# Performance work log

Hardware: AMD Instinct MI355X
Metric: run time of the kernel (lower is better)

## Reference

```python
import jax, jax.numpy as jnp
import numpy as np

C = 1024  # in_channels
B, SQ, SKV = 4, 2048, 2048


def setup_inputs() -> dict:
    key = jax.random.key(0)
    ks = jax.random.split(key, 10)
    s = 1.0 / np.sqrt(C)
    return {
        "x": jax.random.normal(ks[0], (B, SQ, C), jnp.float32),
        "content_embeddings": jax.random.normal(ks[1], (B, SKV, C), jnp.float32),
        "Wq": jax.random.normal(ks[2], (C, C), jnp.float32) * s,
        "bq": jnp.zeros((C,), jnp.float32),
        "Wk": jax.random.normal(ks[3], (C, C), jnp.float32) * s,
        "bk": jnp.zeros((C,), jnp.float32),
        "Wv": jax.random.normal(ks[4], (C, C), jnp.float32) * s,
        "bv": jnp.zeros((C,), jnp.float32),
        "Wo": jax.random.normal(ks[5], (C, C), jnp.float32) * s,
        "bo": jnp.zeros((C,), jnp.float32),
    }


def reference(x, content_embeddings, Wq, bq, Wk, bk, Wv, bv, Wo, bo):
    # torch Linear: y = x @ W.T + b
    queries = x @ Wq.T + bq                    # [B, SQ, C]
    keys = content_embeddings @ Wk.T + bk      # [B, SKV, C]
    values = content_embeddings @ Wv.T + bv    # [B, SKV, C]
    scale = 1.0 / jnp.sqrt(jnp.asarray(C, x.dtype))
    scores = jnp.einsum("bqc,bkc->bqk", queries, keys) * scale  # [B, SQ, SKV]
    attn = jax.nn.softmax(scores, axis=-1)
    attended = jnp.einsum("bqk,bkc->bqc", attn, values)         # [B, SQ, C]
    out = x + attended
    return out @ Wo.T + bo
```

## Files before the change

### kernel.cpp

```cpp
#include <hip/hip_runtime.h>


typedef __attribute__((ext_vector_type(8))) short short8;
typedef __attribute__((ext_vector_type(8))) unsigned short ushort8;
typedef __attribute__((ext_vector_type(4))) unsigned short ushort4v;
typedef __attribute__((ext_vector_type(4))) float f32x4;

__device__ __forceinline__ float b2f(unsigned short u) {
  union { unsigned int i; float f; } x;
  x.i = ((unsigned int)u) << 16;
  return x.f;
}
__device__ __forceinline__ unsigned short f2b(float f) {
  union { float f; unsigned int i; } x;
  x.f = f;
  unsigned int i = x.i;
  i += 0x7fffu + ((i >> 16) & 1u);
  return (unsigned short)(i >> 16);
}

__device__ __forceinline__ void async_copy16(const void* g, void* l) {
  __builtin_amdgcn_global_load_lds(
      (const __attribute__((address_space(1))) unsigned int*)g,
      (__attribute__((address_space(3))) unsigned int*)l, 16, 0, 0);
}

__global__ void detect_fmt(const unsigned short* __restrict__ x, int* flag) {
  __shared__ int cnt;
  if (threadIdx.x == 0) cnt = 0;
  __syncthreads();
  int c = 0;
  for (int i = threadIdx.x * 2; i < 8192; i += 512) {
    unsigned e = (x[i] >> 7) & 0xFF;
    if (e >= 0x90) ++c;
  }
  atomicAdd(&cnt, c);
  __syncthreads();
  if (threadIdx.x == 0) *flag = (cnt > 64) ? 1 : 0;
}

struct CvtArgs { const void* src[10]; };

__global__ __launch_bounds__(256) void convert_all(
    CvtArgs a, unsigned short* __restrict__ dst, const int* __restrict__ flag) {
  const bool f32 = (*flag != 0);
  const long nchunk = 2621952;
  for (long c = blockIdx.x * 256L + threadIdx.x; c < nchunk;
       c += 1024L * 256) {
    const long flat = c * 8;
    int t; long off;
    if      (flat < 8388608)  { t = 0; off = 0; }
    else if (flat < 16777216) { t = 1; off = 8388608; }
    else if (flat < 17825792) { t = 2; off = 16777216; }
    else if (flat < 17826816) { t = 3; off = 17825792; }
    else if (flat < 18875392) { t = 4; off = 17826816; }
    else if (flat < 18876416) { t = 5; off = 18875392; }
    else if (flat < 19924992) { t = 6; off = 18876416; }
    else if (flat < 19926016) { t = 7; off = 19924992; }
    else if (flat < 20974592) { t = 8; off = 19926016; }
    else                      { t = 9; off = 20974592; }
    const long li = flat - off;
    if (f32) {
      const float* s = (const float*)a.src[t] + li;
      const f32x4 lo = *(const f32x4*)s;
      const f32x4 hi = *(const f32x4*)(s + 4);
      ushort8 o;
      o[0] = f2b(lo[0]); o[1] = f2b(lo[1]); o[2] = f2b(lo[2]); o[3] = f2b(lo[3]);
      o[4] = f2b(hi[0]); o[5] = f2b(hi[1]); o[6] = f2b(hi[2]); o[7] = f2b(hi[3]);
      *(ushort8*)(dst + flat) = o;
    } else {
      *(ushort8*)(dst + flat) =
          *(const ushort8*)((const unsigned short*)a.src[t] + li);
    }
  }
}

#define MODE_BIAS 0
#define MODE_RES  2
#define MODE_SB   3
#define MODE_OUT  4

__device__ __forceinline__ void xcd_swizzle(int gx, int gy, int& bx, int& by) {
  const int L = blockIdx.y * gx + blockIdx.x;
  const int r = L & 7, m = L >> 3;
  bx = m % gx;
  by = r * (gy >> 3) + m / gx;
}

template <int MODE, int KU>
__device__ __forceinline__ void gemm_core(
    const unsigned short* __restrict__ A, const unsigned short* __restrict__ B,
    void* __restrict__ C, const unsigned short* __restrict__ bias,
    const unsigned short* __restrict__ Res, const int* __restrict__ flg,
    int N, int K, float scale, int bx, int by, int vt) {
  __shared__ __align__(16) unsigned short As[KU * 128 * 32];
  __shared__ __align__(16) unsigned short Bs[KU * 128 * 32];
  const int tid = threadIdx.x;
  const int wave = tid >> 6, lane = tid & 63;
  const int wm = wave >> 1, wn = wave & 1;
  const int quad = lane >> 4, lrow = lane & 15;

  const long arow0 = (long)by * 128 + (tid >> 2);
  const long brow0 = (long)bx * 128 + (tid >> 2);
  const int cstg = (tid & 3) * 8;
  const unsigned short* ag0 = A + arow0 * K + cstg;
  const unsigned short* ag1 = ag0 + 64L * K;
  const unsigned short* bg0 = B + brow0 * K + cstg;
  const unsigned short* bg1 = bg0 + 64L * K;
  char* lA0 = (char*)As + tid * 16;
  char* lA1 = (char*)As + (256 + tid) * 16;
  char* lB0 = (char*)Bs + tid * 16;
  char* lB1 = (char*)Bs + (256 + tid) * 16;

  f32x4 acc[4][4];
#pragma unroll
  for (int i = 0; i < 4; ++i)
#pragma unroll
    for (int j = 0; j < 4; ++j) acc[i][j] = (f32x4){0.f, 0.f, 0.f, 0.f};

  for (int kt = 0; kt < K; kt += 32 * KU) {
#pragma unroll
    for (int u = 0; u < KU; ++u) {
      async_copy16(ag0 + kt + u * 32, lA0 + u * 8192);
      async_copy16(ag1 + kt + u * 32, lA1 + u * 8192);
      async_copy16(bg0 + kt + u * 32, lB0 + u * 8192);
      async_copy16(bg1 + kt + u * 32, lB1 + u * 8192);
    }
    __syncthreads();
#pragma unroll
    for (int u = 0; u < KU; ++u) {
      const unsigned short* Au = As + u * 4096;
      const unsigned short* Bu = Bs + u * 4096;
      short8 af[4], bfr[4];
#pragma unroll
      for (int i = 0; i < 4; ++i)
        af[i] = *(const short8*)(Au + (wm * 64 + i * 16 + lrow) * 32 + quad * 8);
#pragma unroll
      for (int j = 0; j < 4; ++j)
        bfr[j] =
            *(const short8*)(Bu + (wn * 64 + j * 16 + lrow) * 32 + quad * 8);
#pragma unroll
      for (int i = 0; i < 4; ++i)
#pragma unroll
        for (int j = 0; j < 4; ++j)
          acc[i][j] = __builtin_amdgcn_mfma_f32_16x16x32_bf16(
              af[i], bfr[j], acc[i][j], 0, 0, 0);
    }
    __syncthreads();
  }

  const bool f32out = (MODE == MODE_OUT) ? (*flg != 0) : false;
#pragma unroll
  for (int i = 0; i < 4; ++i) {
    const long row = (long)by * 128 + wm * 64 + i * 16 + quad * 4;
#pragma unroll
    for (int j = 0; j < 4; ++j) {
      const long col = (long)bx * 128 + wn * 64 + j * 16 + lrow;
      if (MODE == MODE_BIAS && vt) {
        const float bb = b2f(bias[col]);
        ushort4v pk;
#pragma unroll
        for (int r = 0; r < 4; ++r) pk[r] = f2b(acc[i][j][r] + bb);
        const long b = row >> 11, kvr = row & 2047;
        *(ushort4v*)((unsigned short*)C + b * 2097152 + col * 2048 + kvr) = pk;
        continue;
      }
#pragma unroll
      for (int r = 0; r < 4; ++r) {
        const float v = acc[i][j][r];
        const long idx = (row + r) * N + col;
        if (MODE == MODE_BIAS) {
          ((unsigned short*)C)[idx] = f2b(v + b2f(bias[col]));
        } else if (MODE == MODE_SB) {
          ((unsigned short*)C)[idx] = f2b(v * scale);
        } else if (MODE == MODE_RES) {
          ((unsigned short*)C)[idx] = f2b(v + b2f(Res[idx]));
        } else {
          const float o = v + b2f(bias[col]);
          if (f32out) ((float*)C)[idx] = o;
          else        ((unsigned short*)C)[idx] = f2b(o);
        }
      }
    }
  }
}

template <int MODE, int KU>
__global__ __launch_bounds__(256, 2) void gemm_nt(
    const unsigned short* __restrict__ A, const unsigned short* __restrict__ B,
    void* __restrict__ C, const unsigned short* __restrict__ bias,
    const unsigned short* __restrict__ Res, const int* __restrict__ flg,
    int N, int K, float scale, long sA, long sB, long sC, long sR) {
  const int bz = blockIdx.z;
  int bx, by;
  xcd_swizzle(gridDim.x, gridDim.y, bx, by);
  const unsigned short* Rb = (MODE == MODE_RES) ? Res + bz * sR : nullptr;
  void* Cb = (MODE == MODE_OUT) ? (void*)((char*)C)
                                : (void*)((unsigned short*)C + bz * sC);
  gemm_core<MODE, KU>(A + bz * sA, B + bz * sB, Cb, bias, Rb, flg, N, K, scale,
                      bx, by, 0);
}

template <int MODE>
__device__ __forceinline__ void gemm256_core(
    const unsigned short* __restrict__ A, const unsigned short* __restrict__ B,
    void* __restrict__ C, const unsigned short* __restrict__ bias,
    const unsigned short* __restrict__ Res, const int* __restrict__ flg,
    int N, int K, float scale, int bx, int by, int vt) {
  __shared__ __align__(16) unsigned short lds[65536];
  const int tid = threadIdx.x;
  const int wave = tid >> 6, lane = tid & 63;
  const int wm = wave >> 2, wn = wave & 3;
  const int quad = lane >> 4, lrow = lane & 15;
  const int NT = K >> 6;

  const int srow = tid >> 3;
  const int sch = (tid & 7) ^ (srow & 7);
  const unsigned short* gA = A + (long)(by * 256 + srow) * K + sch * 8;
  const unsigned short* gB = B + (long)(bx * 256 + srow) * K + sch * 8;
  char* const ldst = (char*)lds + tid * 16;

  auto stageA = [&](int ts, int h) {
    const unsigned short* g = gA + (long)h * 128 * K + ts * 64;
    char* l = ldst + (ts & 1) * 32768 + h * 16384;
    async_copy16(g, l);
    async_copy16(g + (long)64 * K, l + 8192);
  };
  auto stageB = [&](int ts, int h) {
    const unsigned short* g = gB + (long)h * 128 * K + ts * 64;
    char* l = ldst + 65536 + (ts & 1) * 32768 + h * 16384;
    async_copy16(g, l);
    async_copy16(g + (long)64 * K, l + 8192);
  };

  const int chk0 = ((quad) ^ (lrow & 7)) << 3;
  const int chk1 = ((4 + quad) ^ (lrow & 7)) << 3;

  f32x4 acc[8][4];
#pragma unroll
  for (int i = 0; i < 8; ++i)
#pragma unroll
    for (int j = 0; j < 4; ++j) acc[i][j] = (f32x4){0.f, 0.f, 0.f, 0.f};

  stageB(0, 0); stageB(0, 1); stageA(0, 0); stageA(0, 1);
  stageB(1, 0); stageB(1, 1);
  asm volatile("s_waitcnt vmcnt(4)" ::: "memory");
  __builtin_amdgcn_s_barrier();

  for (int t = 0; t < NT; ++t) {
    const unsigned short* Au = lds + (t & 1) * 16384 + (wm * 128 + lrow) * 64;
    const unsigned short* Bu =
        lds + 32768 + (t & 1) * 16384 + (wn * 64 + lrow) * 64;
    short8 a[4][2], blo[2][2], bhi[2][2];

#pragma unroll
    for (int i = 0; i < 4; ++i) {
      a[i][0] = *(const short8*)(Au + i * 1024 + chk0);
      a[i][1] = *(const short8*)(Au + i * 1024 + chk1);
    }
#pragma unroll
    for (int j = 0; j < 2; ++j) {
      blo[j][0] = *(const short8*)(Bu + j * 1024 + chk0);
      blo[j][1] = *(const short8*)(Bu + j * 1024 + chk1);
    }
    if (t + 1 < NT) stageA(t + 1, 0);
    __builtin_amdgcn_s_barrier();
    asm volatile("s_waitcnt lgkmcnt(0)" ::: "memory");
    __builtin_amdgcn_sched_barrier(0);
    __builtin_amdgcn_s_setprio(1);
#pragma unroll
    for (int i = 0; i < 4; ++i)
#pragma unroll
      for (int j = 0; j < 2; ++j) {
        acc[i][j] = __builtin_amdgcn_mfma_f32_16x16x32_bf16(
            a[i][0], blo[j][0], acc[i][j], 0, 0, 0);
        acc[i][j] = __builtin_amdgcn_mfma_f32_16x16x32_bf16(
            a[i][1], blo[j][1], acc[i][j], 0, 0, 0);
      }
    __builtin_amdgcn_s_setprio(0);
    __builtin_amdgcn_s_barrier();

#pragma unroll
    for (int j = 0; j < 2; ++j) {
      bhi[j][0] = *(const short8*)(Bu + (j + 2) * 1024 + chk0);
      bhi[j][1] = *(const short8*)(Bu + (j + 2) * 1024 + chk1);
    }
    if (t + 1 < NT) stageA(t + 1, 1);
    __builtin_amdgcn_s_barrier();
    asm volatile("s_waitcnt lgkmcnt(0)" ::: "memory");
    __builtin_amdgcn_sched_barrier(0);
    __builtin_amdgcn_s_setprio(1);
#pragma unroll
    for (int i = 0; i < 4; ++i)
#pragma unroll
      for (int j = 0; j < 2; ++j) {
        acc[i][j + 2] = __builtin_amdgcn_mfma_f32_16x16x32_bf16(
            a[i][0], bhi[j][0], acc[i][j + 2], 0, 0, 0);
        acc[i][j + 2] = __builtin_amdgcn_mfma_f32_16x16x32_bf16(
            a[i][1], bhi[j][1], acc[i][j + 2], 0, 0, 0);
      }
    __builtin_amdgcn_s_setprio(0);
    __builtin_amdgcn_s_barrier();

#pragma unroll
    for (int i = 0; i < 4; ++i) {
      a[i][0] = *(const short8*)(Au + (i + 4) * 1024 + chk0);
      a[i][1] = *(const short8*)(Au + (i + 4) * 1024 + chk1);
    }
    if (t + 2 < NT) stageB(t + 2, 0);
    __builtin_amdgcn_s_barrier();
    asm volatile("s_waitcnt lgkmcnt(0)" ::: "memory");
    __builtin_amdgcn_sched_barrier(0);
    __builtin_amdgcn_s_setprio(1);
#pragma unroll
    for (int i = 0; i < 4; ++i)
#pragma unroll
      for (int j = 0; j < 2; ++j) {
        acc[i + 4][j + 2] = __builtin_amdgcn_mfma_f32_16x16x32_bf16(
            a[i][0], bhi[j][0], acc[i + 4][j + 2], 0, 0, 0);
        acc[i + 4][j + 2] = __builtin_amdgcn_mfma_f32_16x16x32_bf16(
            a[i][1], bhi[j][1], acc[i + 4][j + 2], 0, 0, 0);
      }
    __builtin_amdgcn_s_setprio(0);
    __builtin_amdgcn_s_barrier();

    if (t + 2 < NT) stageB(t + 2, 1);
    __builtin_amdgcn_s_barrier();
    __builtin_amdgcn_s_setprio(1);
#pragma unroll
    for (int i = 0; i < 4; ++i)
#pragma unroll
      for (int j = 0; j < 2; ++j) {
        acc[i + 4][j] = __builtin_amdgcn_mfma_f32_16x16x32_bf16(
            a[i][0], blo[j][0], acc[i + 4][j], 0, 0, 0);
        acc[i + 4][j] = __builtin_amdgcn_mfma_f32_16x16x32_bf16(
            a[i][1], blo[j][1], acc[i + 4][j], 0, 0, 0);
      }
    __builtin_amdgcn_s_setprio(0);
    if (t + 2 < NT) {
      asm volatile("s_waitcnt vmcnt(4)" ::: "memory");
    } else {
      asm volatile("s_waitcnt vmcnt(0)" ::: "memory");
    }
    __builtin_amdgcn_s_barrier();
  }

  const bool f32out = (MODE == MODE_OUT) ? (*flg != 0) : false;
  float bb[4];
  if (MODE == MODE_BIAS || MODE == MODE_OUT) {
#pragma unroll
    for (int j = 0; j < 4; ++j)
      bb[j] = b2f(bias[(long)bx * 256 + wn * 64 + j * 16 + lrow]);
  }
#pragma unroll
  for (int i = 0; i < 8; ++i) {
    const long row = (long)by * 256 + wm * 128 + i * 16 + quad * 4;
#pragma unroll
    for (int j = 0; j < 4; ++j) {
      const long col = (long)bx * 256 + wn * 64 + j * 16 + lrow;
      if (MODE == MODE_BIAS && vt) {
        ushort4v pk;
#pragma unroll
        for (int r = 0; r < 4; ++r) pk[r] = f2b(acc[i][j][r] + bb[j]);
        const long b = row >> 11, kvr = row & 2047;
        *(ushort4v*)((unsigned short*)C + b * 2097152 + col * 2048 + kvr) = pk;
        continue;
      }
#pragma unroll
      for (int r = 0; r < 4; ++r) {
        const float v = acc[i][j][r];
        const long idx = (row + r) * N + col;
        if (MODE == MODE_BIAS) {
          ((unsigned short*)C)[idx] = f2b(v + bb[j]);
        } else if (MODE == MODE_SB) {
          ((unsigned short*)C)[idx] = f2b(v * scale);
        } else if (MODE == MODE_RES) {
          ((unsigned short*)C)[idx] = f2b(v + b2f(Res[idx]));
        } else {
          const float o = v + bb[j];
          if (f32out) ((float*)C)[idx] = o;
          else        ((unsigned short*)C)[idx] = f2b(o);
        }
      }
    }
  }
}

template <int MODE>
__global__ __launch_bounds__(512, 2) void gemm_nt256(
    const unsigned short* __restrict__ A, const unsigned short* __restrict__ B,
    void* __restrict__ C, const unsigned short* __restrict__ bias,
    const unsigned short* __restrict__ Res, const int* __restrict__ flg,
    int N, int K, float scale, long sA, long sB, long sC, long sR) {
  const int bz = blockIdx.z;
  int bx, by;
  xcd_swizzle(gridDim.x, gridDim.y, bx, by);
  const unsigned short* Rb = (MODE == MODE_RES) ? Res + bz * sR : nullptr;
  void* Cb = (MODE == MODE_OUT) ? (void*)((char*)C)
                                : (void*)((unsigned short*)C + bz * sC);
  gemm256_core<MODE>(A + bz * sA, B + bz * sB, Cb, bias, Rb, flg, N, K, scale,
                     bx, by, 0);
}

struct QkvArgs {
  const unsigned short* A[3];
  const unsigned short* B[3];
  unsigned short* C[3];
  const unsigned short* bias[3];
};
__global__ __launch_bounds__(512, 2) void gemm_qkv(QkvArgs a, int N, int K) {
  const int z = blockIdx.z;
  int bx, by;
  xcd_swizzle(gridDim.x, gridDim.y, bx, by);
  gemm256_core<MODE_BIAS>(a.A[z], a.B[z], a.C[z], a.bias[z], nullptr, nullptr,
                          N, K, 1.f, bx, by, z == 2 ? 1 : 0);
}

__global__ __launch_bounds__(256) void softmax_rows(
    unsigned short* __restrict__ SP) {
  unsigned short* s = SP + blockIdx.x * 2048L;
  const int tid = threadIdx.x;
  const ushort8 raw = *(const ushort8*)(s + tid * 8);
  float v[8];
#pragma unroll
  for (int i = 0; i < 8; ++i) v[i] = b2f(raw[i]);
  float m = v[0];
#pragma unroll
  for (int i = 1; i < 8; ++i) m = fmaxf(m, v[i]);
#pragma unroll
  for (int off = 32; off > 0; off >>= 1) m = fmaxf(m, __shfl_xor(m, off));
  __shared__ float redm[4], reds[4];
  if ((tid & 63) == 0) redm[tid >> 6] = m;
  __syncthreads();
  m = fmaxf(fmaxf(redm[0], redm[1]), fmaxf(redm[2], redm[3]));
  float sum = 0.f;
#pragma unroll
  for (int i = 0; i < 8; ++i) {
    v[i] = __expf(v[i] - m);
    sum += v[i];
  }
#pragma unroll
  for (int off = 32; off > 0; off >>= 1) sum += __shfl_xor(sum, off);
  if ((tid & 63) == 0) reds[tid >> 6] = sum;
  __syncthreads();
  sum = reds[0] + reds[1] + reds[2] + reds[3];
  const float inv = 1.0f / sum;
  ushort8 o;
#pragma unroll
  for (int i = 0; i < 8; ++i) o[i] = f2b(v[i] * inv);
  *(ushort8*)(s + tid * 8) = o;
}

extern "C" void kernel_launch(void* const* d_in, const int* in_sizes, int n_in,
                              void* d_out, int out_size, void* d_ws,
                              size_t ws_size, hipStream_t stream) {
  char* ws = (char*)d_ws;
  const long MB = 1 << 20;
  unsigned short* C0  = (unsigned short*)ws;
  unsigned short* xb  = C0;
  unsigned short* ceb = C0 + 8388608;
  unsigned short* Wqb = C0 + 16777216;
  unsigned short* bqb = C0 + 17825792;
  unsigned short* Wkb = C0 + 17826816;
  unsigned short* bkb = C0 + 18875392;
  unsigned short* Wvb = C0 + 18876416;
  unsigned short* bvb = C0 + 19924992;
  unsigned short* Wob = C0 + 19926016;
  unsigned short* bob = C0 + 20974592;
  int*            flg = (int*)(ws + 41 * MB);
  unsigned short* Q   = (unsigned short*)(ws + 42 * MB);
  unsigned short* Kp  = (unsigned short*)(ws + 58 * MB);
  unsigned short* Vt  = (unsigned short*)(ws + 74 * MB);
  unsigned short* S   = (unsigned short*)(ws + 90 * MB);
  unsigned short* Ar  = Kp;

  const float scale = 0.03125f;

  detect_fmt<<<dim3(1), dim3(256), 0, stream>>>((const unsigned short*)d_in[0],
                                                flg);
  CvtArgs ca;
  for (int i = 0; i < 10; ++i) ca.src[i] = d_in[i];
  convert_all<<<dim3(1024), dim3(256), 0, stream>>>(ca, C0, flg);

  QkvArgs qa;
  qa.A[0] = xb;  qa.A[1] = ceb; qa.A[2] = ceb;
  qa.B[0] = Wqb; qa.B[1] = Wkb; qa.B[2] = Wvb;
  qa.C[0] = Q;   qa.C[1] = Kp;  qa.C[2] = Vt;
  qa.bias[0] = bqb; qa.bias[1] = bkb; qa.bias[2] = bvb;
  gemm_qkv<<<dim3(4, 32, 3), dim3(512), 0, stream>>>(qa, 1024, 1024);

  gemm_nt256<MODE_SB><<<dim3(8, 8, 4), dim3(512), 0, stream>>>(
      Q, Kp, S, nullptr, nullptr, nullptr, 2048, 1024, scale,
      2048L * 1024, 2048L * 1024, 2048L * 2048, 0);

  softmax_rows<<<dim3(8192), dim3(256), 0, stream>>>(S);

  gemm_nt<MODE_RES, 2><<<dim3(8, 16, 4), dim3(256), 0, stream>>>(
      S, Vt, Ar, nullptr, xb, nullptr, 1024, 2048, 1.f,
      2048L * 2048, 1024L * 2048, 2048L * 1024, 2048L * 1024);

  gemm_nt<MODE_OUT, 2><<<dim3(8, 64, 1), dim3(256), 0, stream>>>(
      Ar, Wob, d_out, bob, nullptr, flg, 1024, 1024, 1.f, 0, 0, 0, 0);
}
```

Measured before the change: 330.8 us.

## Restructure GEMM main loop to one prefetch stage with K-split LDS fragments

Replaces the 8-phase ping-pong main loop, which had many block barriers and a two-tile-deep B prefetch, with a single-stage prefetch. All A and B tiles for step t+1 are issued at once, and each step ends with one vmcnt(0) wait and a barrier. LDS fragment reads are split by K half, and partial lgkmcnt waits let MFMAs start while later fragments are still loading. This removes most intra-iteration s_barriers. In exchange, global-load latency is exposed at the end of each step because the loop waits on vmcnt(0) with no deeper prefetch.

After: 327.8 us. No clear change (-0.9%).

```diff
diff --git a/kernel.cpp b/kernel.cpp
--- a/kernel.cpp
+++ b/kernel.cpp
@@ -242,106 +242,96 @@
 #pragma unroll
     for (int j = 0; j < 4; ++j) acc[i][j] = (f32x4){0.f, 0.f, 0.f, 0.f};
 
-  stageB(0, 0); stageB(0, 1); stageA(0, 0); stageA(0, 1);
-  stageB(1, 0); stageB(1, 1);
-  asm volatile("s_waitcnt vmcnt(4)" ::: "memory");
+  stageA(0, 0); stageA(0, 1); stageB(0, 0); stageB(0, 1);
+  asm volatile("s_waitcnt vmcnt(0)" ::: "memory");
   __builtin_amdgcn_s_barrier();
 
   for (int t = 0; t < NT; ++t) {
     const unsigned short* Au = lds + (t & 1) * 16384 + (wm * 128 + lrow) * 64;
     const unsigned short* Bu =
         lds + 32768 + (t & 1) * 16384 + (wn * 64 + lrow) * 64;
-    short8 a[4][2], blo[2][2], bhi[2][2];
-
-#pragma unroll
-    for (int i = 0; i < 4; ++i) {
-      a[i][0] = *(const short8*)(Au + i * 1024 + chk0);
-      a[i][1] = *(const short8*)(Au + i * 1024 + chk1);
-    }
-#pragma unroll
-    for (int j = 0; j < 2; ++j) {
-      blo[j][0] = *(const short8*)(Bu + j * 1024 + chk0);
-      blo[j][1] = *(const short8*)(Bu + j * 1024 + chk1);
-    }
-    if (t + 1 < NT) stageA(t + 1, 0);
-    __builtin_amdgcn_s_barrier();
+    short8 alo[4][2], ahi[4][2], b[4][2];
+
+#pragma unroll
+    for (int i = 0; i < 4; ++i)
+      alo[i][0] = *(const short8*)(Au + i * 1024 + chk0);
+#pragma unroll
+    for (int j = 0; j < 4; ++j)
+      b[j][0] = *(const short8*)(Bu + j * 1024 + chk0);
+    __builtin_amdgcn_sched_barrier(0);
+#pragma unroll
+    for (int i = 0; i < 4; ++i)
+      alo[i][1] = *(const short8*)(Au + i * 1024 + chk1);
+#pragma unroll
+    for (int j = 0; j < 4; ++j)
+      b[j][1] = *(const short8*)(Bu + j * 1024 + chk1);
+    __builtin_amdgcn_sched_barrier(0);
+
+    if (t + 1 < NT) {
+      stageA(t + 1, 0); stageA(t + 1, 1);
+      stageB(t + 1, 0); stageB(t + 1, 1);
+    }
+    __builtin_amdgcn_sched_barrier(0);
+
+    asm volatile("s_waitcnt lgkmcnt(8)" ::: "memory");
+    __builtin_amdgcn_sched_barrier(0);
+    __builtin_amdgcn_s_setprio(1);
+#pragma unroll
+    for (int i = 0; i < 4; ++i)
+#pragma unroll
+      for (int j = 0; j < 4; ++j)
+        acc[i][j] = __builtin_amdgcn_mfma_f32_16x16x32_bf16(
+            alo[i][0], b[j][0], acc[i][j], 0, 0, 0);
+    __builtin_amdgcn_s_setprio(0);
+    __builtin_amdgcn_sched_barrier(0);
+
+#pragma unroll
+    for (int i = 0; i < 4; ++i)
+      ahi[i][0] = *(const short8*)(Au + (i + 4) * 1024 + chk0);
+    __builtin_amdgcn_sched_barrier(0);
+
+    asm volatile("s_waitcnt lgkmcnt(4)" ::: "memory");
+    __builtin_amdgcn_sched_barrier(0);
+    __builtin_amdgcn_s_setprio(1);
+#pragma unroll
+    for (int i = 0; i < 4; ++i)
+#pragma unroll
+      for (int j = 0; j < 4; ++j)
+        acc[i][j] = __builtin_amdgcn_mfma_f32_16x16x32_bf16(
+            alo[i][1], b[j][1], acc[i][j], 0, 0, 0);
+    __builtin_amdgcn_s_setprio(0);
+    __builtin_amdgcn_sched_barrier(0);
+
+#pragma unroll
+    for (int i = 0; i < 4; ++i)
+      ahi[i][1] = *(const short8*)(Au + (i + 4) * 1024 + chk1);
+    __builtin_amdgcn_sched_barrier(0);
+
+    asm volatile("s_waitcnt lgkmcnt(4)" ::: "memory");
+    __builtin_amdgcn_sched_barrier(0);
+    __builtin_amdgcn_s_setprio(1);
+#pragma unroll
+    for (int i = 0; i < 4; ++i)
+#pragma unroll
+      for (int j = 0; j < 4; ++j)
+        acc[i + 4][j] = __builtin_amdgcn_mfma_f32_16x16x32_bf16(
+            ahi[i][0], b[j][0], acc[i + 4][j], 0, 0, 0);
+    __builtin_amdgcn_s_setprio(0);
+    __builtin_amdgcn_sched_barrier(0);
+
     asm volatile("s_waitcnt lgkmcnt(0)" ::: "memory");
     __builtin_amdgcn_sched_barrier(0);
     __builtin_amdgcn_s_setprio(1);
 #pragma unroll
     for (int i = 0; i < 4; ++i)
 #pragma unroll
-      for (int j = 0; j < 2; ++j) {
-        acc[i][j] = __builtin_amdgcn_mfma_f32_16x16x32_bf16(
-            a[i][0], blo[j][0], acc[i][j], 0, 0, 0);
-        acc[i][j] = __builtin_amdgcn_mfma_f32_16x16x32_bf16(
-            a[i][1], blo[j][1], acc[i][j], 0, 0, 0);
-      }
+      for (int j = 0; j < 4; ++j)
+        acc[i + 4][j] = __builtin_amdgcn_mfma_f32_16x16x32_bf16(
+            ahi[i][1], b[j][1], acc[i + 4][j], 0, 0, 0);
     __builtin_amdgcn_s_setprio(0);
-    __builtin_amdgcn_s_barrier();
-
-#pragma unroll
-    for (int j = 0; j < 2; ++j) {
-      bhi[j][0] = *(const short8*)(Bu + (j + 2) * 1024 + chk0);
-      bhi[j][1] = *(const short8*)(Bu + (j + 2) * 1024 + chk1);
-    }
-    if (t + 1 < NT) stageA(t + 1, 1);
-    __builtin_amdgcn_s_barrier();
-    asm volatile("s_waitcnt lgkmcnt(0)" ::: "memory");
-    __builtin_amdgcn_sched_barrier(0);
-    __builtin_amdgcn_s_setprio(1);
-#pragma unroll
-    for (int i = 0; i < 4; ++i)
-#pragma unroll
-      for (int j = 0; j < 2; ++j) {
-        acc[i][j + 2] = __builtin_amdgcn_mfma_f32_16x16x32_bf16(
-            a[i][0], bhi[j][0], acc[i][j + 2], 0, 0, 0);
-        acc[i][j + 2] = __builtin_amdgcn_mfma_f32_16x16x32_bf16(
-            a[i][1], bhi[j][1], acc[i][j + 2], 0, 0, 0);
-      }
-    __builtin_amdgcn_s_setprio(0);
-    __builtin_amdgcn_s_barrier();
-
-#pragma unroll
-    for (int i = 0; i < 4; ++i) {
-      a[i][0] = *(const short8*)(Au + (i + 4) * 1024 + chk0);
-      a[i][1] = *(const short8*)(Au + (i + 4) * 1024 + chk1);
-    }
-    if (t + 2 < NT) stageB(t + 2, 0);
-    __builtin_amdgcn_s_barrier();
-    asm volatile("s_waitcnt lgkmcnt(0)" ::: "memory");
-    __builtin_amdgcn_sched_barrier(0);
-    __builtin_amdgcn_s_setprio(1);
-#pragma unroll
-    for (int i = 0; i < 4; ++i)
-#pragma unroll
-      for (int j = 0; j < 2; ++j) {
-        acc[i + 4][j + 2] = __builtin_amdgcn_mfma_f32_16x16x32_bf16(
-            a[i][0], bhi[j][0], acc[i + 4][j + 2], 0, 0, 0);
-        acc[i + 4][j + 2] = __builtin_amdgcn_mfma_f32_16x16x32_bf16(
-            a[i][1], bhi[j][1], acc[i + 4][j + 2], 0, 0, 0);
-      }
-    __builtin_amdgcn_s_setprio(0);
-    __builtin_amdgcn_s_barrier();
-
-    if (t + 2 < NT) stageB(t + 2, 1);
-    __builtin_amdgcn_s_barrier();
-    __builtin_amdgcn_s_setprio(1);
-#pragma unroll
-    for (int i = 0; i < 4; ++i)
-#pragma unroll
-      for (int j = 0; j < 2; ++j) {
-        acc[i + 4][j] = __builtin_amdgcn_mfma_f32_16x16x32_bf16(
-            a[i][0], blo[j][0], acc[i + 4][j], 0, 0, 0);
-        acc[i + 4][j] = __builtin_amdgcn_mfma_f32_16x16x32_bf16(
-            a[i][1], blo[j][1], acc[i + 4][j], 0, 0, 0);
-      }
-    __builtin_amdgcn_s_setprio(0);
-    if (t + 2 < NT) {
-      asm volatile("s_waitcnt vmcnt(4)" ::: "memory");
-    } else {
-      asm volatile("s_waitcnt vmcnt(0)" ::: "memory");
-    }
+    __builtin_amdgcn_sched_barrier(0);
+
+    asm volatile("s_waitcnt vmcnt(0)" ::: "memory");
     __builtin_amdgcn_s_barrier();
   }
 
```
